# Optimization experiments

Hardware: AMD Instinct MI355X
Metric: run time of the kernel (lower is better)

Reference implementation:

```python
import jax, jax.numpy as jnp
import numpy as np

EMBED_DIM = 1024
N_HEADS = 16
HEAD_DIM = EMBED_DIM // N_HEADS
N_CATS = 5
SCALE = float(np.sqrt(HEAD_DIM))


def setup_inputs() -> dict:
    key = jax.random.key(0)
    ks = jax.random.split(key, 16)
    B, S = 2, 2048
    inp = {
        "query": jax.random.normal(ks[0], (B, S, EMBED_DIM), jnp.float32),
        "key_": jax.random.normal(ks[1], (B, S, EMBED_DIM), jnp.float32),
        "value": jax.random.normal(ks[2], (B, S, EMBED_DIM), jnp.float32),
        "responses": jax.random.randint(ks[3], (B, S), 0, N_CATS),
        "mask": jnp.ones((B, S, S), jnp.int32),
        # Linear params (torch convention: y = x @ W.T + b)
        "Wq": jax.random.normal(ks[4], (EMBED_DIM, EMBED_DIM), jnp.float32) * 0.02,
        "bq": jnp.zeros((EMBED_DIM,), jnp.float32),
        "Wk": jax.random.normal(ks[5], (EMBED_DIM, EMBED_DIM), jnp.float32) * 0.02,
        "bk": jnp.zeros((EMBED_DIM,), jnp.float32),
        "Wv": jax.random.normal(ks[6], (EMBED_DIM, EMBED_DIM), jnp.float32) * 0.02,
        "bv": jnp.zeros((EMBED_DIM,), jnp.float32),
        "Wo": jax.random.normal(ks[7], (EMBED_DIM, EMBED_DIM), jnp.float32) * 0.02,
        "bo": jnp.zeros((EMBED_DIM,), jnp.float32),
        # qwk_modulation: Linear(1, n_heads)
        "Wm": jax.random.normal(ks[8], (N_HEADS, 1), jnp.float32) * 0.5,
        "bm": jnp.zeros((N_HEADS,), jnp.float32),
    }
    return inp


def _qwk_matrix():
    i = jnp.arange(N_CATS, dtype=jnp.float32)
    return 1.0 - (i[:, None] - i[None, :]) ** 2 / (N_CATS - 1) ** 2  # [C, C]


def reference(query, key_, value, responses, mask,
              Wq, bq, Wk, bk, Wv, bv, Wo, bo, Wm, bm):
    B, S, E = query.shape
    # projections
    Q = (query @ Wq.T + bq).reshape(B, S, N_HEADS, HEAD_DIM).transpose(0, 2, 1, 3)
    K = (key_ @ Wk.T + bk).reshape(B, S, N_HEADS, HEAD_DIM).transpose(0, 2, 1, 3)
    V = (value @ Wv.T + bv).reshape(B, S, N_HEADS, HEAD_DIM).transpose(0, 2, 1, 3)
    scores = jnp.einsum("bhqd,bhkd->bhqk", Q, K) / SCALE  # [B,H,S,S]
    # QWK ordinal bias: gather pairwise weight, tiny linear 1->H, broadcast-add
    qwk = _qwk_matrix()
    pair = qwk[responses[:, :, None], responses[:, None, :]]  # [B,S,S]
    # Linear(1, n_heads): bias[...,None] @ Wm.T + bm -> [B,S,S,H] -> [B,H,S,S]
    head_bias = pair[:, None, :, :] * Wm[:, 0][None, :, None, None] + bm[None, :, None, None]
    scores = scores + head_bias
    scores = jnp.where(mask[:, None, :, :] == 0, -1e9, scores)
    attn = jax.nn.softmax(scores, axis=-1)
    attended = jnp.einsum("bhqk,bhkd->bhqd", attn, V)
    attended = attended.transpose(0, 2, 1, 3).reshape(B, S, E)
    return attended @ Wo.T + bo
```

## Files before the change

### kernel.cpp

```cpp
#include <hip/hip_runtime.h>
#include <hip/hip_bf16.h>
#include <stdint.h>

#define S_LEN 2048
#define EMB   1024
#define NHEAD 16
#define HDIM  64
#define BATCH 2

typedef __bf16 bf16x8 __attribute__((ext_vector_type(8)));
typedef float  f32x4  __attribute__((ext_vector_type(4)));

__device__ __forceinline__ void gll16(const void* g, void* l) {
  __builtin_amdgcn_global_load_lds(
      (const __attribute__((address_space(1))) void*)g,
      (__attribute__((address_space(3))) void*)l,
      16, 0, 0);
}

__global__ void __launch_bounds__(256) cast_kernel(
    const float* __restrict__ s0, const float* __restrict__ s1, const float* __restrict__ s2,
    const float* __restrict__ s3, const float* __restrict__ s4, const float* __restrict__ s5,
    const float* __restrict__ s6,
    __hip_bfloat16* __restrict__ d0, __hip_bfloat16* __restrict__ d1,
    __hip_bfloat16* __restrict__ d2, __hip_bfloat16* __restrict__ d3,
    __hip_bfloat16* __restrict__ d4, __hip_bfloat16* __restrict__ d5,
    __hip_bfloat16* __restrict__ d6) {
  const int z = blockIdx.y;
  const float* s = (z == 0) ? s0 : (z == 1) ? s1 : (z == 2) ? s2 : (z == 3) ? s3
                 : (z == 4) ? s4 : (z == 5) ? s5 : s6;
  __hip_bfloat16* d = (z == 0) ? d0 : (z == 1) ? d1 : (z == 2) ? d2 : (z == 3) ? d3
                    : (z == 4) ? d4 : (z == 5) ? d5 : d6;
  const int n = (z < 3) ? (BATCH * S_LEN * EMB) : (EMB * EMB);
  const size_t i = ((size_t)blockIdx.x * 256 + threadIdx.x) * 16;
  if (i >= (size_t)n) return;
  __hip_bfloat16 tmp[16];
#pragma unroll
  for (int j = 0; j < 4; ++j) {
    const float4 v = *(const float4*)(s + i + j * 4);
    tmp[j * 4 + 0] = __float2bfloat16(v.x);
    tmp[j * 4 + 1] = __float2bfloat16(v.y);
    tmp[j * 4 + 2] = __float2bfloat16(v.z);
    tmp[j * 4 + 3] = __float2bfloat16(v.w);
  }
  *(bf16x8*)(d + i)     = *(bf16x8*)&tmp[0];
  *(bf16x8*)(d + i + 8) = *(bf16x8*)&tmp[8];
}

__global__ void __launch_bounds__(256) mask_flags_kernel(const int* __restrict__ mask,
                                                         unsigned* __restrict__ flags) {
  const int kt = blockIdx.x, qt = blockIdx.y, b = blockIdx.z;
  const int t = threadIdx.x;
  const int* base = mask + ((size_t)b * S_LEN + (size_t)qt * 64) * S_LEN + (size_t)kt * 128;
  int ok = 1;
#pragma unroll
  for (int p = 0; p < 8; ++p) {
    int idx = p * 256 + t;
    int row = idx >> 5, c4 = idx & 31;
    const int4 v = *(const int4*)(base + (size_t)row * S_LEN + c4 * 4);
    ok &= (v.x != 0) & (v.y != 0) & (v.z != 0) & (v.w != 0);
  }
  unsigned long long bl = __ballot(ok);
  __shared__ unsigned long long bw[4];
  bw[t >> 6] = bl;
  __syncthreads();
  if (t == 0) {
    unsigned all = ((bw[0] & bw[1] & bw[2] & bw[3]) == ~0ull) ? 1u : 0u;
    flags[((size_t)b * 32 + qt) * 16 + kt] = all;
  }
}

__global__ void __launch_bounds__(256, 2)
gemm_kernel(const __hip_bfloat16* __restrict__ A0, const __hip_bfloat16* __restrict__ A1,
            const __hip_bfloat16* __restrict__ A2,
            const __hip_bfloat16* __restrict__ W0, const __hip_bfloat16* __restrict__ W1,
            const __hip_bfloat16* __restrict__ W2,
            const float* __restrict__ b0, const float* __restrict__ b1,
            const float* __restrict__ b2,
            __hip_bfloat16* __restrict__ O0, __hip_bfloat16* __restrict__ O1,
            __hip_bfloat16* __restrict__ O2) {
  __shared__ __align__(16) __hip_bfloat16 As[128 * 32];
  __shared__ __align__(16) __hip_bfloat16 Bs[128 * 32];

  const int z = blockIdx.z;
  const __hip_bfloat16* A  = (z == 0) ? A0 : ((z == 1) ? A1 : A2);
  const __hip_bfloat16* W  = (z == 0) ? W0 : ((z == 1) ? W1 : W2);
  const float* bi          = (z == 0) ? b0 : ((z == 1) ? b1 : b2);
  __hip_bfloat16* O        = (z == 0) ? O0 : ((z == 1) ? O1 : O2);

  const int t = threadIdx.x;
  const int w = t >> 6, lane = t & 63, quad = lane >> 4, l15 = lane & 15;
  const int m0 = blockIdx.y * 128, n0 = blockIdx.x * 128;
  const int wr = w >> 1, wc = w & 1;

  f32x4 acc[4][4];
#pragma unroll
  for (int i = 0; i < 4; ++i)
#pragma unroll
    for (int j = 0; j < 4; ++j) acc[i][j] = (f32x4)0.0f;

  for (int k0 = 0; k0 < EMB; k0 += 32) {
    __syncthreads();
#pragma unroll
    for (int rnd = 0; rnd < 2; ++rnd) {
      int idx = rnd * 256 + t;
      gll16(A + (size_t)(m0 + (idx >> 2)) * EMB + k0 + ((idx & 3) << 3),
            &As[(rnd * 256 + (w << 6)) * 8]);
      gll16(W + (size_t)(n0 + (idx >> 2)) * EMB + k0 + ((idx & 3) << 3),
            &Bs[(rnd * 256 + (w << 6)) * 8]);
    }
    __syncthreads();

    bf16x8 af[4], bfr[4];
#pragma unroll
    for (int i = 0; i < 4; ++i)
      af[i] = *(const bf16x8*)&As[(wr * 64 + i * 16 + l15) * 32 + quad * 8];
#pragma unroll
    for (int j = 0; j < 4; ++j)
      bfr[j] = *(const bf16x8*)&Bs[(wc * 64 + j * 16 + l15) * 32 + quad * 8];
#pragma unroll
    for (int i = 0; i < 4; ++i)
#pragma unroll
      for (int j = 0; j < 4; ++j)
        acc[i][j] = __builtin_amdgcn_mfma_f32_16x16x32_bf16(af[i], bfr[j], acc[i][j], 0, 0, 0);
  }

#pragma unroll
  for (int j = 0; j < 4; ++j) {
    const int ng = n0 + wc * 64 + j * 16 + l15;
    const float bb = bi[ng];
    const int h = ng >> 6, d = ng & 63;
#pragma unroll
    for (int i = 0; i < 4; ++i) {
#pragma unroll
      for (int r = 0; r < 4; ++r) {
        const int mg = m0 + wr * 64 + i * 16 + quad * 4 + r;
        const int b = mg >> 11, s = mg & 2047;
        float v = acc[i][j][r] + bb;
        if (z == 0) {
          O[(((size_t)b * NHEAD + h) * S_LEN + s) * HDIM + d] =
              __float2bfloat16(v * (0.125f * 1.4426950408889634f));
        } else if (z == 1) {
          O[(((size_t)b * NHEAD + h) * S_LEN + s) * HDIM + d] = __float2bfloat16(v);
        } else {
          O[(((size_t)b * NHEAD + h) * HDIM + d) * S_LEN + s] = __float2bfloat16(v);
        }
      }
    }
  }
}

__global__ void __launch_bounds__(256, 2)
gemm_o_kernel(const __hip_bfloat16* __restrict__ A, const __hip_bfloat16* __restrict__ W,
              const float* __restrict__ bi, float* __restrict__ O) {
  __shared__ __align__(16) __hip_bfloat16 As[64 * 32];
  __shared__ __align__(16) __hip_bfloat16 Bs[128 * 32];
  const int t = threadIdx.x;
  const int w = t >> 6, lane = t & 63, quad = lane >> 4, l15 = lane & 15;
  const int m0 = blockIdx.y * 64, n0 = blockIdx.x * 128;
  const int wr = w >> 1, wc = w & 1;

  f32x4 acc[2][4];
#pragma unroll
  for (int i = 0; i < 2; ++i)
#pragma unroll
    for (int j = 0; j < 4; ++j) acc[i][j] = (f32x4)0.0f;

  for (int k0 = 0; k0 < EMB; k0 += 32) {
    __syncthreads();
    gll16(A + (size_t)(m0 + (t >> 2)) * EMB + k0 + ((t & 3) << 3), &As[(w << 6) * 8]);
#pragma unroll
    for (int rnd = 0; rnd < 2; ++rnd) {
      int idx = rnd * 256 + t;
      gll16(W + (size_t)(n0 + (idx >> 2)) * EMB + k0 + ((idx & 3) << 3),
            &Bs[(rnd * 256 + (w << 6)) * 8]);
    }
    __syncthreads();

    bf16x8 af[2], bfr[4];
#pragma unroll
    for (int i = 0; i < 2; ++i)
      af[i] = *(const bf16x8*)&As[(wr * 32 + i * 16 + l15) * 32 + quad * 8];
#pragma unroll
    for (int j = 0; j < 4; ++j)
      bfr[j] = *(const bf16x8*)&Bs[(wc * 64 + j * 16 + l15) * 32 + quad * 8];
#pragma unroll
    for (int i = 0; i < 2; ++i)
#pragma unroll
      for (int j = 0; j < 4; ++j)
        acc[i][j] = __builtin_amdgcn_mfma_f32_16x16x32_bf16(af[i], bfr[j], acc[i][j], 0, 0, 0);
  }

#pragma unroll
  for (int j = 0; j < 4; ++j) {
    const int ng = n0 + wc * 64 + j * 16 + l15;
    const float bb = bi[ng];
#pragma unroll
    for (int i = 0; i < 2; ++i) {
#pragma unroll
      for (int r = 0; r < 4; ++r) {
        const int mg = m0 + wr * 32 + i * 16 + quad * 4 + r;
        O[(size_t)mg * EMB + ng] = acc[i][j][r] + bb;
      }
    }
  }
}

__global__ void __launch_bounds__(256, 4)
flash_kernel(const __hip_bfloat16* __restrict__ qws, const __hip_bfloat16* __restrict__ kws,
             const __hip_bfloat16* __restrict__ vtws, const int* __restrict__ responses,
             const int* __restrict__ mask, const float* __restrict__ Wm,
             const unsigned* __restrict__ flags, __hip_bfloat16* __restrict__ att) {
  __shared__ __align__(16) __hip_bfloat16 KP[128 * 64];
  __shared__ __align__(16) __hip_bfloat16 Vs[64 * 128];
  __shared__ unsigned char rb[S_LEN];
  __shared__ float tab[32];

  const int t = threadIdx.x;
  const int w = t >> 6, lane = t & 63, quad = lane >> 4, l15 = lane & 15;
  const int qt = blockIdx.x, h = blockIdx.y, b = blockIdx.z;
  const int bh = b * NHEAD + h;
  const int q0 = qt * 64;

  if (t < 25) {
    const float c = Wm[h] * (0.0625f * 1.4426950408889634f);
    const int rq = t / 5, rk = t % 5;
    tab[t] = __builtin_amdgcn_exp2f(c * (float)(2 * rq * rk - rk * rk));
  }
#pragma unroll
  for (int i = 0; i < 8; ++i)
    rb[i * 256 + t] = (unsigned char)responses[b * S_LEN + i * 256 + t];

  const __hip_bfloat16* qbase = qws + ((size_t)bh * S_LEN + q0) * HDIM;
  bf16x8 qf[2];
#pragma unroll
  for (int ks = 0; ks < 2; ++ks)
    qf[ks] = *(const bf16x8*)(qbase + (size_t)(w * 16 + l15) * HDIM + ks * 32 + quad * 8);

  int toff[4];
#pragma unroll
  for (int r = 0; r < 4; ++r)
    toff[r] = responses[b * S_LEN + q0 + w * 16 + quad * 4 + r] * 5;

  const __hip_bfloat16* kptr = kws + ((size_t)bh * S_LEN + (t >> 3)) * HDIM +
                               (((t & 7) ^ ((t >> 3) & 7)) << 3);
  const __hip_bfloat16* vptr = vtws + ((size_t)bh * HDIM + (t >> 4)) * S_LEN +
                               (((t & 15) ^ ((t >> 4) & 7)) << 3);

  float lsum[4] = {0.f, 0.f, 0.f, 0.f};
  f32x4 acc_o[4];
#pragma unroll
  for (int dt = 0; dt < 4; ++dt) acc_o[dt] = (f32x4)0.0f;

  for (int kt = 0; kt < S_LEN / 128; ++kt) {
    __syncthreads();
#pragma unroll
    for (int p = 0; p < 4; ++p) {
      gll16(kptr + p * 32 * HDIM,  &KP[(p * 256 + (w << 6)) * 8]);
      gll16(vptr + p * 16 * S_LEN, &Vs[(p * 256 + (w << 6)) * 8]);
    }
    kptr += 128 * HDIM;
    vptr += 128;
    __syncthreads();

    f32x4 sc[8];
#pragma unroll
    for (int ct = 0; ct < 8; ++ct) {
      const int rowk = ct * 16 + l15;
      bf16x8 kf0 = *(const bf16x8*)&KP[rowk * 64 + (((0 + quad) ^ (l15 & 7)) << 3)];
      bf16x8 kf1 = *(const bf16x8*)&KP[rowk * 64 + (((4 + quad) ^ (l15 & 7)) << 3)];
      sc[ct] = __builtin_amdgcn_mfma_f32_16x16x32_bf16(qf[0], kf0, (f32x4)0.0f, 0, 0, 0);
      sc[ct] = __builtin_amdgcn_mfma_f32_16x16x32_bf16(qf[1], kf1, sc[ct], 0, 0, 0);
    }

    int rk8[8];
#pragma unroll
    for (int ct = 0; ct < 8; ++ct) rk8[ct] = rb[kt * 128 + ct * 16 + l15];

    const unsigned fl = flags[((size_t)b * 32 + qt) * 16 + kt];

    __syncthreads();

#pragma unroll
    for (int ct = 0; ct < 8; ++ct) {
      const int cb = (ct << 1) | (l15 >> 3);
#pragma unroll
      for (int r = 0; r < 4; ++r) {
        float p = __builtin_amdgcn_exp2f(sc[ct][r]) * tab[toff[r] + rk8[ct]];
        if (!fl) {
          int mq = mask[((size_t)b * S_LEN + q0 + w * 16 + quad * 4 + r) * S_LEN +
                        kt * 128 + ct * 16 + l15];
          p = mq ? p : 0.0f;
        }
        lsum[r] += p;
        const int prow = w * 16 + quad * 4 + r;
        KP[prow * 128 + ((cb ^ (prow & 7)) << 3) + (l15 & 7)] = __float2bfloat16(p);
      }
    }

#pragma unroll
    for (int kst = 0; kst < 4; ++kst) {
      const int prow = w * 16 + l15;
      bf16x8 pf = *(const bf16x8*)&KP[prow * 128 + ((((kst << 2) + quad) ^ (l15 & 7)) << 3)];
#pragma unroll
      for (int dt = 0; dt < 4; ++dt) {
        const int vrow = dt * 16 + l15;
        bf16x8 vf = *(const bf16x8*)&Vs[vrow * 128 + ((((kst << 2) + quad) ^ (l15 & 7)) << 3)];
        acc_o[dt] = __builtin_amdgcn_mfma_f32_16x16x32_bf16(pf, vf, acc_o[dt], 0, 0, 0);
      }
    }
  }

#pragma unroll
  for (int r = 0; r < 4; ++r) {
#pragma unroll
    for (int off = 1; off < 16; off <<= 1) lsum[r] += __shfl_xor(lsum[r], off, 64);
    lsum[r] = 1.0f / lsum[r];
  }
#pragma unroll
  for (int dt = 0; dt < 4; ++dt) {
#pragma unroll
    for (int r = 0; r < 4; ++r) {
      float v = acc_o[dt][r] * lsum[r];
      att[((size_t)b * S_LEN + q0 + w * 16 + quad * 4 + r) * EMB + h * HDIM + dt * 16 + l15] =
          __float2bfloat16(v);
    }
  }
}

extern "C" void kernel_launch(void* const* d_in, const int* in_sizes, int n_in,
                              void* d_out, int out_size, void* d_ws, size_t ws_size,
                              hipStream_t stream) {
  const float* query = (const float*)d_in[0];
  const float* key_  = (const float*)d_in[1];
  const float* value = (const float*)d_in[2];
  const int* responses = (const int*)d_in[3];
  const int* mask      = (const int*)d_in[4];
  const float* Wq = (const float*)d_in[5];
  const float* bq = (const float*)d_in[6];
  const float* Wk = (const float*)d_in[7];
  const float* bk = (const float*)d_in[8];
  const float* Wv = (const float*)d_in[9];
  const float* bv = (const float*)d_in[10];
  const float* Wo = (const float*)d_in[11];
  const float* bo = (const float*)d_in[12];
  const float* Wm = (const float*)d_in[13];

  __hip_bfloat16* ws = (__hip_bfloat16*)d_ws;
  const size_t NTOK = (size_t)BATCH * S_LEN * EMB;
  const size_t NW   = (size_t)EMB * EMB;
  __hip_bfloat16* qcast = ws;
  __hip_bfloat16* kcast = ws + NTOK;
  __hip_bfloat16* vcast = ws + 2 * NTOK;
  __hip_bfloat16* wqb   = ws + 3 * NTOK;
  __hip_bfloat16* wkb   = wqb + NW;
  __hip_bfloat16* wvb   = wqb + 2 * NW;
  __hip_bfloat16* wob   = wqb + 3 * NW;
  __hip_bfloat16* qws   = wqb + 4 * NW;
  __hip_bfloat16* kws   = qws + NTOK;
  __hip_bfloat16* vtws  = qws + 2 * NTOK;
  __hip_bfloat16* att   = qws + 3 * NTOK;
  unsigned* flags       = (unsigned*)(qws + 4 * NTOK);
  float* out            = (float*)d_out;

  cast_kernel<<<dim3(1024, 7), 256, 0, stream>>>(query, key_, value, Wq, Wk, Wv, Wo,
                                                 qcast, kcast, vcast, wqb, wkb, wvb, wob);
  mask_flags_kernel<<<dim3(16, 32, 2), 256, 0, stream>>>(mask, flags);
  gemm_kernel<<<dim3(8, 32, 3), 256, 0, stream>>>(qcast, kcast, vcast, wqb, wkb, wvb,
                                                  bq, bk, bv, qws, kws, vtws);
  flash_kernel<<<dim3(32, 16, 2), 256, 0, stream>>>(qws, kws, vtws, responses, mask,
                                                    Wm, flags, att);
  gemm_o_kernel<<<dim3(8, 64), 256, 0, stream>>>(att, wob, bo, out);
}
```

Before: 295.2 us.

## Keep P in registers via transposed QK MFMA and prepacked V layout

```diff
diff --git a/kernel.cpp b/kernel.cpp
--- a/kernel.cpp
+++ b/kernel.cpp
@@ -18,21 +18,44 @@
       16, 0, 0);
 }
 
-__global__ void __launch_bounds__(256) cast_kernel(
+__global__ void __launch_bounds__(256) cast_mask_kernel(
     const float* __restrict__ s0, const float* __restrict__ s1, const float* __restrict__ s2,
     const float* __restrict__ s3, const float* __restrict__ s4, const float* __restrict__ s5,
     const float* __restrict__ s6,
     __hip_bfloat16* __restrict__ d0, __hip_bfloat16* __restrict__ d1,
     __hip_bfloat16* __restrict__ d2, __hip_bfloat16* __restrict__ d3,
     __hip_bfloat16* __restrict__ d4, __hip_bfloat16* __restrict__ d5,
-    __hip_bfloat16* __restrict__ d6) {
+    __hip_bfloat16* __restrict__ d6,
+    const int* __restrict__ mask, unsigned* __restrict__ flags) {
   const int z = blockIdx.y;
+  const int t = threadIdx.x;
+  if (z == 7) {
+    const int kt = blockIdx.x & 15, qt = (blockIdx.x >> 4) & 31, b = (int)blockIdx.x >> 9;
+    const int* base = mask + ((size_t)b * S_LEN + (size_t)qt * 64) * S_LEN + (size_t)kt * 128;
+    int ok = 1;
+#pragma unroll
+    for (int p = 0; p < 8; ++p) {
+      int idx = p * 256 + t;
+      int row = idx >> 5, c4 = idx & 31;
+      const int4 v = *(const int4*)(base + (size_t)row * S_LEN + c4 * 4);
+      ok &= (v.x != 0) & (v.y != 0) & (v.z != 0) & (v.w != 0);
+    }
+    unsigned long long bl = __ballot(ok);
+    __shared__ unsigned long long bw[4];
+    bw[t >> 6] = bl;
+    __syncthreads();
+    if (t == 0) {
+      unsigned all = ((bw[0] & bw[1] & bw[2] & bw[3]) == ~0ull) ? 1u : 0u;
+      flags[((size_t)b * 32 + qt) * 16 + kt] = all;
+    }
+    return;
+  }
   const float* s = (z == 0) ? s0 : (z == 1) ? s1 : (z == 2) ? s2 : (z == 3) ? s3
                  : (z == 4) ? s4 : (z == 5) ? s5 : s6;
   __hip_bfloat16* d = (z == 0) ? d0 : (z == 1) ? d1 : (z == 2) ? d2 : (z == 3) ? d3
                     : (z == 4) ? d4 : (z == 5) ? d5 : d6;
   const int n = (z < 3) ? (BATCH * S_LEN * EMB) : (EMB * EMB);
-  const size_t i = ((size_t)blockIdx.x * 256 + threadIdx.x) * 16;
+  const size_t i = ((size_t)blockIdx.x * 256 + t) * 16;
   if (i >= (size_t)n) return;
   __hip_bfloat16 tmp[16];
 #pragma unroll
@@ -45,29 +68,6 @@
   }
   *(bf16x8*)(d + i)     = *(bf16x8*)&tmp[0];
   *(bf16x8*)(d + i + 8) = *(bf16x8*)&tmp[8];
-}
-
-__global__ void __launch_bounds__(256) mask_flags_kernel(const int* __restrict__ mask,
-                                                         unsigned* __restrict__ flags) {
-  const int kt = blockIdx.x, qt = blockIdx.y, b = blockIdx.z;
-  const int t = threadIdx.x;
-  const int* base = mask + ((size_t)b * S_LEN + (size_t)qt * 64) * S_LEN + (size_t)kt * 128;
-  int ok = 1;
-#pragma unroll
-  for (int p = 0; p < 8; ++p) {
-    int idx = p * 256 + t;
-    int row = idx >> 5, c4 = idx & 31;
-    const int4 v = *(const int4*)(base + (size_t)row * S_LEN + c4 * 4);
-    ok &= (v.x != 0) & (v.y != 0) & (v.z != 0) & (v.w != 0);
-  }
-  unsigned long long bl = __ballot(ok);
-  __shared__ unsigned long long bw[4];
-  bw[t >> 6] = bl;
-  __syncthreads();
-  if (t == 0) {
-    unsigned all = ((bw[0] & bw[1] & bw[2] & bw[3]) == ~0ull) ? 1u : 0u;
-    flags[((size_t)b * 32 + qt) * 16 + kt] = all;
-  }
 }
 
 __global__ void __launch_bounds__(256, 2)
@@ -143,7 +143,10 @@
         } else if (z == 1) {
           O[(((size_t)b * NHEAD + h) * S_LEN + s) * HDIM + d] = __float2bfloat16(v);
         } else {
-          O[(((size_t)b * NHEAD + h) * HDIM + d) * S_LEN + s] = __float2bfloat16(v);
+          const size_t idx = (size_t)(b * NHEAD + h) * 131072 + (size_t)(s >> 7) * 8192 +
+                             (size_t)((((s >> 5) & 3) * 4 + ((s >> 2) & 3)) * 64 + d) * 8 +
+                             ((s >> 4) & 1) * 4 + (s & 3);
+          O[idx] = __float2bfloat16(v);
         }
       }
     }
@@ -208,13 +211,12 @@
 
 __global__ void __launch_bounds__(256, 4)
 flash_kernel(const __hip_bfloat16* __restrict__ qws, const __hip_bfloat16* __restrict__ kws,
-             const __hip_bfloat16* __restrict__ vtws, const int* __restrict__ responses,
+             const __hip_bfloat16* __restrict__ vpk, const int* __restrict__ responses,
              const int* __restrict__ mask, const float* __restrict__ Wm,
              const unsigned* __restrict__ flags, __hip_bfloat16* __restrict__ att) {
-  __shared__ __align__(16) __hip_bfloat16 KP[128 * 64];
-  __shared__ __align__(16) __hip_bfloat16 Vs[64 * 128];
+  __shared__ __align__(16) __hip_bfloat16 Ks[128 * 64];
+  __shared__ __align__(16) __hip_bfloat16 Vs[8192];
   __shared__ unsigned char rb[S_LEN];
-  __shared__ float tab[32];
 
   const int t = threadIdx.x;
   const int w = t >> 6, lane = t & 63, quad = lane >> 4, l15 = lane & 15;
@@ -222,11 +224,6 @@
   const int bh = b * NHEAD + h;
   const int q0 = qt * 64;
 
-  if (t < 25) {
-    const float c = Wm[h] * (0.0625f * 1.4426950408889634f);
-    const int rq = t / 5, rk = t % 5;
-    tab[t] = __builtin_amdgcn_exp2f(c * (float)(2 * rq * rk - rk * rk));
-  }
 #pragma unroll
   for (int i = 0; i < 8; ++i)
     rb[i * 256 + t] = (unsigned char)responses[b * S_LEN + i * 256 + t];
@@ -237,17 +234,15 @@
   for (int ks = 0; ks < 2; ++ks)
     qf[ks] = *(const bf16x8*)(qbase + (size_t)(w * 16 + l15) * HDIM + ks * 32 + quad * 8);
 
-  int toff[4];
-#pragma unroll
-  for (int r = 0; r < 4; ++r)
-    toff[r] = responses[b * S_LEN + q0 + w * 16 + quad * 4 + r] * 5;
+  const float c = Wm[h] * (0.0625f * 1.4426950408889634f);
+  const float rqf = (float)responses[b * S_LEN + q0 + w * 16 + l15];
+  const float A2 = 2.0f * c * rqf;
 
   const __hip_bfloat16* kptr = kws + ((size_t)bh * S_LEN + (t >> 3)) * HDIM +
                                (((t & 7) ^ ((t >> 3) & 7)) << 3);
-  const __hip_bfloat16* vptr = vtws + ((size_t)bh * HDIM + (t >> 4)) * S_LEN +
-                               (((t & 15) ^ ((t >> 4) & 7)) << 3);
-
-  float lsum[4] = {0.f, 0.f, 0.f, 0.f};
+  const __hip_bfloat16* vptr = vpk + (size_t)bh * 131072 + (size_t)t * 8;
+
+  float lsum = 0.0f;
   f32x4 acc_o[4];
 #pragma unroll
   for (int dt = 0; dt < 4; ++dt) acc_o[dt] = (f32x4)0.0f;
@@ -256,72 +251,66 @@
     __syncthreads();
 #pragma unroll
     for (int p = 0; p < 4; ++p) {
-      gll16(kptr + p * 32 * HDIM,  &KP[(p * 256 + (w << 6)) * 8]);
-      gll16(vptr + p * 16 * S_LEN, &Vs[(p * 256 + (w << 6)) * 8]);
+      gll16(kptr + p * 32 * HDIM, &Ks[(p * 256 + (w << 6)) * 8]);
+      gll16(vptr + p * 2048,      &Vs[(p * 256 + (w << 6)) * 8]);
     }
     kptr += 128 * HDIM;
-    vptr += 128;
-    __syncthreads();
-
-    f32x4 sc[8];
+    vptr += 8192;
+    __syncthreads();
+
+    const unsigned fl = flags[((size_t)b * 32 + qt) * 16 + kt];
+
+    bf16x8 pfr[4];
 #pragma unroll
     for (int ct = 0; ct < 8; ++ct) {
       const int rowk = ct * 16 + l15;
-      bf16x8 kf0 = *(const bf16x8*)&KP[rowk * 64 + (((0 + quad) ^ (l15 & 7)) << 3)];
-      bf16x8 kf1 = *(const bf16x8*)&KP[rowk * 64 + (((4 + quad) ^ (l15 & 7)) << 3)];
-      sc[ct] = __builtin_amdgcn_mfma_f32_16x16x32_bf16(qf[0], kf0, (f32x4)0.0f, 0, 0, 0);
-      sc[ct] = __builtin_amdgcn_mfma_f32_16x16x32_bf16(qf[1], kf1, sc[ct], 0, 0, 0);
-    }
-
-    int rk8[8];
-#pragma unroll
-    for (int ct = 0; ct < 8; ++ct) rk8[ct] = rb[kt * 128 + ct * 16 + l15];
-
-    const unsigned fl = flags[((size_t)b * 32 + qt) * 16 + kt];
-
-    __syncthreads();
-
-#pragma unroll
-    for (int ct = 0; ct < 8; ++ct) {
-      const int cb = (ct << 1) | (l15 >> 3);
+      bf16x8 kf0 = *(const bf16x8*)&Ks[rowk * 64 + ((quad ^ (l15 & 7)) << 3)];
+      bf16x8 kf1 = *(const bf16x8*)&Ks[rowk * 64 + (((4 + quad) ^ (l15 & 7)) << 3)];
+      f32x4 sc = __builtin_amdgcn_mfma_f32_16x16x32_bf16(kf0, qf[0], (f32x4)0.0f, 0, 0, 0);
+      sc = __builtin_amdgcn_mfma_f32_16x16x32_bf16(kf1, qf[1], sc, 0, 0, 0);
+
+      const unsigned ru = *(const unsigned*)&rb[kt * 128 + ct * 16 + quad * 4];
+
+      __hip_bfloat16 pb[4];
 #pragma unroll
       for (int r = 0; r < 4; ++r) {
-        float p = __builtin_amdgcn_exp2f(sc[ct][r]) * tab[toff[r] + rk8[ct]];
+        const float rkf = (float)((ru >> (8 * r)) & 255u);
+        const float tt = fmaf(-c, rkf, A2);
+        const float sb = fmaf(rkf, tt, sc[r]);
+        float p = __builtin_amdgcn_exp2f(sb);
         if (!fl) {
-          int mq = mask[((size_t)b * S_LEN + q0 + w * 16 + quad * 4 + r) * S_LEN +
-                        kt * 128 + ct * 16 + l15];
+          int mq = mask[((size_t)b * S_LEN + q0 + w * 16 + l15) * S_LEN +
+                        kt * 128 + ct * 16 + quad * 4 + r];
           p = mq ? p : 0.0f;
         }
-        lsum[r] += p;
-        const int prow = w * 16 + quad * 4 + r;
-        KP[prow * 128 + ((cb ^ (prow & 7)) << 3) + (l15 & 7)] = __float2bfloat16(p);
+        lsum += p;
+        pb[r] = __float2bfloat16(p);
       }
-    }
-
-#pragma unroll
-    for (int kst = 0; kst < 4; ++kst) {
-      const int prow = w * 16 + l15;
-      bf16x8 pf = *(const bf16x8*)&KP[prow * 128 + ((((kst << 2) + quad) ^ (l15 & 7)) << 3)];
+      __hip_bfloat16* half = (__hip_bfloat16*)&pfr[ct >> 1] + (ct & 1) * 4;
+      half[0] = pb[0]; half[1] = pb[1]; half[2] = pb[2]; half[3] = pb[3];
+    }
+
+#pragma unroll
+    for (int ct2 = 0; ct2 < 4; ++ct2) {
 #pragma unroll
       for (int dt = 0; dt < 4; ++dt) {
-        const int vrow = dt * 16 + l15;
-        bf16x8 vf = *(const bf16x8*)&Vs[vrow * 128 + ((((kst << 2) + quad) ^ (l15 & 7)) << 3)];
-        acc_o[dt] = __builtin_amdgcn_mfma_f32_16x16x32_bf16(pf, vf, acc_o[dt], 0, 0, 0);
+        bf16x8 vv = *(const bf16x8*)&Vs[((((ct2 << 2) + quad) << 6) + (dt << 4) + l15) << 3];
+        acc_o[dt] = __builtin_amdgcn_mfma_f32_16x16x32_bf16(pfr[ct2], vv, acc_o[dt], 0, 0, 0);
       }
     }
   }
 
-#pragma unroll
-  for (int r = 0; r < 4; ++r) {
-#pragma unroll
-    for (int off = 1; off < 16; off <<= 1) lsum[r] += __shfl_xor(lsum[r], off, 64);
-    lsum[r] = 1.0f / lsum[r];
-  }
+  lsum += __shfl_xor(lsum, 16, 64);
+  lsum += __shfl_xor(lsum, 32, 64);
+  float inv[4];
+#pragma unroll
+  for (int r = 0; r < 4; ++r) inv[r] = 1.0f / __shfl(lsum, quad * 4 + r, 64);
+
 #pragma unroll
   for (int dt = 0; dt < 4; ++dt) {
 #pragma unroll
     for (int r = 0; r < 4; ++r) {
-      float v = acc_o[dt][r] * lsum[r];
+      float v = acc_o[dt][r] * inv[r];
       att[((size_t)b * S_LEN + q0 + w * 16 + quad * 4 + r) * EMB + h * HDIM + dt * 16 + l15] =
           __float2bfloat16(v);
     }
@@ -358,17 +347,17 @@
   __hip_bfloat16* wob   = wqb + 3 * NW;
   __hip_bfloat16* qws   = wqb + 4 * NW;
   __hip_bfloat16* kws   = qws + NTOK;
-  __hip_bfloat16* vtws  = qws + 2 * NTOK;
+  __hip_bfloat16* vpk   = qws + 2 * NTOK;
   __hip_bfloat16* att   = qws + 3 * NTOK;
   unsigned* flags       = (unsigned*)(qws + 4 * NTOK);
   float* out            = (float*)d_out;
 
-  cast_kernel<<<dim3(1024, 7), 256, 0, stream>>>(query, key_, value, Wq, Wk, Wv, Wo,
-                                                 qcast, kcast, vcast, wqb, wkb, wvb, wob);
-  mask_flags_kernel<<<dim3(16, 32, 2), 256, 0, stream>>>(mask, flags);
+  cast_mask_kernel<<<dim3(1024, 8), 256, 0, stream>>>(
+      query, key_, value, Wq, Wk, Wv, Wo,
+      qcast, kcast, vcast, wqb, wkb, wvb, wob, mask, flags);
   gemm_kernel<<<dim3(8, 32, 3), 256, 0, stream>>>(qcast, kcast, vcast, wqb, wkb, wvb,
-                                                  bq, bk, bv, qws, kws, vtws);
-  flash_kernel<<<dim3(32, 16, 2), 256, 0, stream>>>(qws, kws, vtws, responses, mask,
+                                                  bq, bk, bv, qws, kws, vpk);
+  flash_kernel<<<dim3(32, 16, 2), 256, 0, stream>>>(qws, kws, vpk, responses, mask,
                                                     Wm, flags, att);
   gemm_o_kernel<<<dim3(8, 64), 256, 0, stream>>>(att, wob, bo, out);
 }
```

New measurement: 262.9 us. 10.9% less time.
